# Kernel optimization log

Hardware: AMD Instinct MI355X
Metric: run time of the kernel (lower is better)

The kernel has to match this reference:

```python
import jax, jax.numpy as jnp
import numpy as np

N, IN_DIM, D, H, E, L = 50000, 16, 128, 256, 800000, 3


def setup_inputs() -> dict:
    key = jax.random.key(0)
    ks = jax.random.split(key, 32)
    s = 0.1
    inp = {
        "x": jax.random.normal(ks[0], (N, IN_DIM), dtype=jnp.float32),
        "edge_index": jax.random.randint(ks[1], (2, E), 0, N, dtype=jnp.int64),
        "enc_W": s * jax.random.normal(ks[2], (IN_DIM, D), dtype=jnp.float32),
        "enc_b": jnp.zeros((D,), jnp.float32),
        "msg_W1": s * jax.random.normal(ks[3], (L, 2 * D, H), dtype=jnp.float32),
        "msg_b1": jnp.zeros((L, H), jnp.float32),
        "msg_W2": s * jax.random.normal(ks[4], (L, H, H), dtype=jnp.float32),
        "msg_b2": jnp.zeros((L, H), jnp.float32),
        "msg_W3": s * jax.random.normal(ks[5], (L, H, D), dtype=jnp.float32),
        "msg_b3": jnp.zeros((L, D), jnp.float32),
        "gru_Wih": s * jax.random.normal(ks[6], (L, D, 3 * D), dtype=jnp.float32),
        "gru_Whh": s * jax.random.normal(ks[7], (L, D, 3 * D), dtype=jnp.float32),
        "gru_bih": jnp.zeros((L, 3 * D), jnp.float32),
        "gru_bhh": jnp.zeros((L, 3 * D), jnp.float32),
        "dec_W1": s * jax.random.normal(ks[8], (D, H), dtype=jnp.float32),
        "dec_b1": jnp.zeros((H,), jnp.float32),
        "dec_W2": s * jax.random.normal(ks[9], (H, H), dtype=jnp.float32),
        "dec_b2": jnp.zeros((H,), jnp.float32),
        "dec_W3": s * jax.random.normal(ks[10], (H, 1), dtype=jnp.float32),
        "dec_b3": jnp.zeros((1,), jnp.float32),
    }
    return inp


def reference(x, edge_index, enc_W, enc_b, msg_W1, msg_b1, msg_W2, msg_b2,
              msg_W3, msg_b3, gru_Wih, gru_Whh, gru_bih, gru_bhh,
              dec_W1, dec_b1, dec_W2, dec_b2, dec_W3, dec_b3):
    n = x.shape[0]
    d = enc_W.shape[1]
    # add self loops (PyG add_self_loops)
    loops = jnp.arange(n, dtype=edge_index.dtype)
    src = jnp.concatenate([edge_index[0], loops])  # x_j
    tgt = jnp.concatenate([edge_index[1], loops])  # x_i / aggregation bucket
    counts = jax.ops.segment_sum(jnp.ones_like(tgt, dtype=x.dtype), tgt, num_segments=n)
    # Encoder: Linear + Tanh
    h = jnp.tanh(x @ enc_W + enc_b)
    for l in range(msg_W1.shape[0]):
        # message: MLP(concat(x_i, x_j))  -> [E+N, d]
        m = jnp.concatenate([h[tgt], h[src]], axis=-1)
        m = jnp.tanh(m @ msg_W1[l] + msg_b1[l])
        m = jnp.tanh(m @ msg_W2[l] + msg_b2[l])
        m = m @ msg_W3[l] + msg_b3[l]
        # aggregate: scatter-mean into target nodes
        agg = jax.ops.segment_sum(m, tgt, num_segments=n) / counts[:, None]
        # update: GRUCell(input=agg, hidden=h)
        gi = agg @ gru_Wih[l] + gru_bih[l]
        gh = h @ gru_Whh[l] + gru_bhh[l]
        r = jax.nn.sigmoid(gi[:, :d] + gh[:, :d])
        z = jax.nn.sigmoid(gi[:, d:2 * d] + gh[:, d:2 * d])
        nn_ = jnp.tanh(gi[:, 2 * d:] + r * gh[:, 2 * d:])
        h = (1.0 - z) * nn_ + z * h
    # Decoder: Linear+Tanh, Linear+Tanh, Linear
    o = jnp.tanh(h @ dec_W1 + dec_b1)
    o = jnp.tanh(o @ dec_W2 + dec_b2)
    o = o @ dec_W3 + dec_b3  # [n, 1]
    return o[:, 0]  # x.view(-1, num_nodes).squeeze(0)
```

## Files before the change

### kernel.cpp

```cpp
#include <hip/hip_runtime.h>
#include <math.h>

#define NN 50000
#define NP 50048
#define NB 782
#define IN_DIM 16
#define DD 128
#define HH 256
#define NE 800000
#define NLAYERS 3
#define ET (NE + NN)
#define EBLK 13282

typedef unsigned short ushort_t;
typedef unsigned int uint_t;
typedef __attribute__((ext_vector_type(8))) short bf16x8;
typedef __attribute__((ext_vector_type(4))) float f32x4;

__device__ __forceinline__ float fast_tanh(float x) {
  float e = __builtin_amdgcn_exp2f(x * 2.88539008177793f);
  float r = __builtin_amdgcn_rcpf(e + 1.0f);
  return fmaf(-2.0f, r, 1.0f);
}

__device__ __forceinline__ float fast_sigmoid(float x) {
  float e = __builtin_amdgcn_exp2f(x * -1.44269504088896f);
  return __builtin_amdgcn_rcpf(e + 1.0f);
}

__device__ __forceinline__ ushort_t f2bf(float f) {
  uint_t u = __float_as_uint(f);
  u += 0x7FFFu + ((u >> 16) & 1u);
  return (ushort_t)(u >> 16);
}

__device__ __forceinline__ uint_t pack2bf(float lo, float hi) {
#if __has_builtin(__builtin_amdgcn_cvt_pk_bf16_f32)
  auto v = __builtin_amdgcn_cvt_pk_bf16_f32(lo, hi);
  uint_t r;
  __builtin_memcpy(&r, &v, 4);
  return r;
#else
  return (uint_t)f2bf(lo) | ((uint_t)f2bf(hi) << 16);
#endif
}

__device__ __forceinline__ float bflo(uint_t d) { return __uint_as_float(d << 16); }
__device__ __forceinline__ float bfhi(uint_t d) { return __uint_as_float(d & 0xFFFF0000u); }



__global__ void deg_kernel(const int* __restrict__ etgt, int* __restrict__ deg) {
  int e = blockIdx.x * blockDim.x + threadIdx.x;
  if (e >= ET) return;
  int tg = (e < NE) ? etgt[e] : (e - NE);
  atomicAdd(&deg[tg], 1);
}

__global__ __launch_bounds__(1024) void scan_kernel(const int* __restrict__ deg,
                                                    int* __restrict__ cursor,
                                                    float* __restrict__ invc) {
  __shared__ int wsum[16];
  __shared__ int carry_s;
  const int t = threadIdx.x;
  const int lane = t & 63, wid = t >> 6;
  if (t == 0) carry_s = 0;
  __syncthreads();
  for (int base = 0; base < NN; base += 1024) {
    int i = base + t;
    int d = (i < NN) ? deg[i] : 0;
    int v = d;
#pragma unroll
    for (int off = 1; off < 64; off <<= 1) {
      int u = __shfl_up(v, off);
      if (lane >= off) v += u;
    }
    if (lane == 63) wsum[wid] = v;
    __syncthreads();
    int woff = 0;
    for (int k = 0; k < wid; ++k) woff += wsum[k];
    int incl = v + woff;
    int carry = carry_s;
    __syncthreads();
    if (i < NN) {
      cursor[i] = carry + incl - d;
      invc[i] = 1.0f / (float)d;
    }
    if (t == 1023) carry_s = carry + incl;
    __syncthreads();
  }
}

__global__ void scatter_kernel(const int* __restrict__ esrc, const int* __restrict__ etgt,
                               int* __restrict__ cursor, int* __restrict__ sSrc,
                               int* __restrict__ sTgt) {
  int e = blockIdx.x * blockDim.x + threadIdx.x;
  if (e >= ET) return;
  int s, tg;
  if (e < NE) { s = esrc[e]; tg = etgt[e]; }
  else        { s = e - NE;  tg = s; }
  int pos = atomicAdd(&cursor[tg], 1);
  sSrc[pos] = s;
  sTgt[pos] = tg;
}


__global__ void encoder_kernel(const float* __restrict__ x, const float* __restrict__ W,
                               const float* __restrict__ b, float* __restrict__ h,
                               ushort_t* __restrict__ hbf) {
  int idx = blockIdx.x * blockDim.x + threadIdx.x;
  if (idx >= NN * DD) return;
  int n = idx >> 7, j = idx & (DD - 1);
  const float* xr = x + n * IN_DIM;
  float acc = b[j];
#pragma unroll
  for (int k = 0; k < IN_DIM; ++k) acc = fmaf(xr[k], W[k * DD + j], acc);
  float v = fast_tanh(acc);
  h[idx] = v;
  const int ct = (n >> 4) & 3, mr = n & 15, ks = j >> 5, q = (j >> 3) & 3, jj = j & 7;
  hbf[(size_t)(n >> 6) * 8192 + (((ct * 4 + ks) * 64) + q * 16 + mr) * 8 + jj] = f2bf(v);
}

__global__ void pack_kernel(const float* __restrict__ W, ushort_t* __restrict__ out,
                            int M, int kbsh, int ngrp, int srcStride, int outStride) {
  int tid = blockIdx.x * blockDim.x + threadIdx.x;
  if (tid >= ngrp * 64) return;
  const float* Ws = W + (size_t)blockIdx.y * srcStride;
  ushort_t* os = out + (size_t)blockIdx.y * outStride;
  int lane = tid & 63, g = tid >> 6;
  int ks = g & ((1 << kbsh) - 1);
  int rt = g >> kbsh;
  int m = rt * 16 + (lane & 15);
  int k0 = ks * 32 + ((lane >> 4) << 3);
  uint_t p[4];
#pragma unroll
  for (int d = 0; d < 4; ++d)
    p[d] = pack2bf(Ws[(size_t)(k0 + 2 * d) * M + m], Ws[(size_t)(k0 + 2 * d + 1) * M + m]);
  uint4 o;
  o.x = p[0]; o.y = p[1]; o.z = p[2]; o.w = p[3];
  *(uint4*)(os + (size_t)tid * 8) = o;
}

__global__ __launch_bounds__(256) void proj_kernel(
    const ushort_t* __restrict__ hbf, const ushort_t* __restrict__ W1p,
    const float* __restrict__ b1, ushort_t* __restrict__ Ptb, ushort_t* __restrict__ Psb) {
  const int t = threadIdx.x, blk = blockIdx.x;
  const int w = t >> 6, l = t & 63, quad = l >> 4, col = l & 15;
  const ushort_t* hb = hbf + (size_t)blk * 8192;
#pragma unroll
  for (int half = 0; half < 2; ++half) {
    f32x4 acc[4][4];
#pragma unroll
    for (int m = 0; m < 4; ++m)
#pragma unroll
      for (int ct = 0; ct < 4; ++ct) acc[m][ct] = (f32x4){0.f, 0.f, 0.f, 0.f};
#pragma unroll
    for (int ks = 0; ks < 4; ++ks) {
      bf16x8 af[4];
#pragma unroll
      for (int m = 0; m < 4; ++m)
        af[m] = *(const bf16x8*)&W1p[((size_t)((w * 4 + m) * 8 + half * 4 + ks) * 64 + l) * 8];
#pragma unroll
      for (int ct = 0; ct < 4; ++ct) {
        bf16x8 bf = *(const bf16x8*)&hb[((ct * 4 + ks) * 64 + l) * 8];
#pragma unroll
        for (int m = 0; m < 4; ++m)
          acc[m][ct] = __builtin_amdgcn_mfma_f32_16x16x32_bf16(af[m], bf, acc[m][ct], 0, 0, 0);
      }
    }
    ushort_t* out = half ? Psb : Ptb;
#pragma unroll
    for (int m = 0; m < 4; ++m) {
      const int o0 = (w * 4 + m) * 16 + quad * 4;
      f32x4 bb = (f32x4){0.f, 0.f, 0.f, 0.f};
      if (half == 0) bb = *(const f32x4*)(b1 + o0);
#pragma unroll
      for (int ct = 0; ct < 4; ++ct) {
        const size_t node = (size_t)blk * 64 + ct * 16 + col;
        uint2 d;
        d.x = pack2bf(acc[m][ct][0] + bb[0], acc[m][ct][1] + bb[1]);
        d.y = pack2bf(acc[m][ct][2] + bb[2], acc[m][ct][3] + bb[3]);
        *(uint2*)&out[node * HH + o0] = d;
      }
    }
  }
}

__global__ __launch_bounds__(256, 4) void edge_kernel(
    const int* __restrict__ sSrc, const int* __restrict__ sTgt,
    const ushort_t* __restrict__ Ptb, const ushort_t* __restrict__ Psb,
    const ushort_t* __restrict__ W2p, const float* __restrict__ b2,
    const ushort_t* __restrict__ W3p, const float* __restrict__ b3,
    const float* __restrict__ invc, float* __restrict__ agg) {
  __shared__ __align__(16) float vBf[64 * 132];
  __shared__ int sIdx[64];
  __shared__ int tIdx[64];
  ushort_t* vB = (ushort_t*)vBf;
  const int t = threadIdx.x;
  const int e0 = blockIdx.x * 64;
  if (t < 64) {
    int e = e0 + t;
    int s = 0, tg = -1;
    if (e < ET) { s = sSrc[e]; tg = sTgt[e]; }
    sIdx[t] = s;
    tIdx[t] = tg;
  }
  __syncthreads();
  {
    const int el = t & 63, c = t >> 6;
    int tg = tIdx[el]; if (tg < 0) tg = 0;
    const int s = sIdx[el];
    const uint4* pt = (const uint4*)(Ptb + (size_t)tg * HH + c * 64);
    const uint4* ps = (const uint4*)(Psb + (size_t)s * HH + c * 64);
    const int ct = el >> 4, mr = el & 15;
#pragma unroll
    for (int g = 0; g < 8; ++g) {
      uint4 av = pt[g];
      uint4 bv = ps[g];
      uint_t ad[4] = {av.x, av.y, av.z, av.w};
      uint_t bd[4] = {bv.x, bv.y, bv.z, bv.w};
      uint_t p[4];
#pragma unroll
      for (int d = 0; d < 4; ++d) {
        float flo = bflo(ad[d]) + bflo(bd[d]);
        float fhi = bfhi(ad[d]) + bfhi(bd[d]);
        p[d] = pack2bf(fast_tanh(flo), fast_tanh(fhi));
      }
      uint4 o;
      o.x = p[0]; o.y = p[1]; o.z = p[2]; o.w = p[3];
      const int ks = c * 2 + (g >> 2);
      const int quad = g & 3;
      *(uint4*)&vB[((ct * 8 + ks) * 64 + quad * 16 + mr) * 8] = o;
    }
  }
  __syncthreads();
  const int w = t >> 6, l = t & 63;
  const int quad = l >> 4, col = l & 15;
  f32x4 acc2[4][4];
#pragma unroll
  for (int rp = 0; rp < 4; ++rp)
#pragma unroll
    for (int ct = 0; ct < 4; ++ct) acc2[rp][ct] = (f32x4){0.f, 0.f, 0.f, 0.f};
#pragma unroll
  for (int ks = 0; ks < 8; ++ks) {
    bf16x8 bfrag[4];
#pragma unroll
    for (int ct = 0; ct < 4; ++ct)
      bfrag[ct] = *(const bf16x8*)&vB[((ct * 8 + ks) * 64 + l) * 8];
#pragma unroll
    for (int rp = 0; rp < 4; ++rp) {
      bf16x8 afrag = *(const bf16x8*)&W2p[((size_t)((w * 4 + rp) * 8 + ks) * 64 + l) * 8];
#pragma unroll
      for (int ct = 0; ct < 4; ++ct)
        acc2[rp][ct] = __builtin_amdgcn_mfma_f32_16x16x32_bf16(afrag, bfrag[ct], acc2[rp][ct], 0, 0, 0);
    }
  }
  __syncthreads();
#pragma unroll
  for (int rp = 0; rp < 4; ++rp) {
    f32x4 bb = *(const f32x4*)(b2 + w * 64 + rp * 16 + quad * 4);
#pragma unroll
    for (int ct = 0; ct < 4; ++ct) {
      uint2 d;
      d.x = pack2bf(fast_tanh(acc2[rp][ct][0] + bb[0]), fast_tanh(acc2[rp][ct][1] + bb[1]));
      d.y = pack2bf(fast_tanh(acc2[rp][ct][2] + bb[2]), fast_tanh(acc2[rp][ct][3] + bb[3]));
      const int gidx = (ct * 8 + w * 2 + (rp >> 1)) * 64 + ((rp & 1) * 2 + (quad >> 1)) * 16 + col;
      *(uint2*)&vB[gidx * 8 + (quad & 1) * 4] = d;
    }
  }
  __syncthreads();
  f32x4 acc3[2][4];
#pragma unroll
  for (int rp = 0; rp < 2; ++rp)
#pragma unroll
    for (int ct = 0; ct < 4; ++ct) acc3[rp][ct] = (f32x4){0.f, 0.f, 0.f, 0.f};
#pragma unroll
  for (int ks = 0; ks < 8; ++ks) {
    bf16x8 bfrag[4];
#pragma unroll
    for (int ct = 0; ct < 4; ++ct)
      bfrag[ct] = *(const bf16x8*)&vB[((ct * 8 + ks) * 64 + l) * 8];
#pragma unroll
    for (int rp = 0; rp < 2; ++rp) {
      bf16x8 afrag = *(const bf16x8*)&W3p[((size_t)((w * 2 + rp) * 8 + ks) * 64 + l) * 8];
#pragma unroll
      for (int ct = 0; ct < 4; ++ct)
        acc3[rp][ct] = __builtin_amdgcn_mfma_f32_16x16x32_bf16(afrag, bfrag[ct], acc3[rp][ct], 0, 0, 0);
    }
  }
  __syncthreads();
  {
#pragma unroll
    for (int rp = 0; rp < 2; ++rp) {
      const int m0 = w * 32 + rp * 16 + quad * 4;
      f32x4 b3v = *(const f32x4*)(b3 + m0);
#pragma unroll
      for (int ct = 0; ct < 4; ++ct) {
        float4 o4;
        o4.x = acc3[rp][ct][0] + b3v[0];
        o4.y = acc3[rp][ct][1] + b3v[1];
        o4.z = acc3[rp][ct][2] + b3v[2];
        o4.w = acc3[rp][ct][3] + b3v[3];
        *(float4*)(vBf + (ct * 16 + col) * 132 + m0) = o4;
      }
    }
  }
  __syncthreads();
  {
    const int j = t & 127;
    const int hb = t >> 7;
    const float* colp = vBf + j;
    int cur = tIdx[hb * 32];
    float a = 0.f;
    for (int e = hb * 32; e < hb * 32 + 32; ++e) {
      int tg = tIdx[e];
      if (tg != cur) {
        if (cur >= 0) atomicAdd(&agg[(size_t)cur * DD + j], a * invc[cur]);
        a = 0.f;
        cur = tg;
      }
      a += colp[e * 132];
    }
    if (cur >= 0) atomicAdd(&agg[(size_t)cur * DD + j], a * invc[cur]);
  }
}

__global__ __launch_bounds__(256, 2) void gru_kernel(
    const float* __restrict__ agg, const float* __restrict__ hg,
    const ushort_t* __restrict__ hbf_in,
    const ushort_t* __restrict__ Wihp, const ushort_t* __restrict__ Whhp,
    const float* __restrict__ bih, const float* __restrict__ bhh,
    float* __restrict__ hg_out, ushort_t* __restrict__ hbf_out,
    int doProj, const ushort_t* __restrict__ W1p, const float* __restrict__ b1,
    ushort_t* __restrict__ Ptb, ushort_t* __restrict__ Psb) {
  __shared__ __align__(16) ushort_t aggF[64 * 128];
  __shared__ __align__(16) float hT[64 * 132];
  __shared__ __align__(16) ushort_t hbfL[64 * 128];
  const int t = threadIdx.x, blk = blockIdx.x;
  const size_t nodeBase = (size_t)blk * 64;
  {
    const int row = t >> 2, c = t & 3;
    const float4* ap = (const float4*)(agg + (nodeBase + row) * DD + c * 32);
    const int ct = row >> 4, mr = row & 15;
#pragma unroll
    for (int g = 0; g < 8; ++g) {
      float4 v = ap[g];
      uint2 d;
      d.x = pack2bf(v.x, v.y);
      d.y = pack2bf(v.z, v.w);
      *(uint2*)&aggF[(((ct * 4 + c) * 64) + (g >> 1) * 16 + mr) * 8 + (g & 1) * 4] = d;
    }
    const float4* hp = (const float4*)(hg + (nodeBase + row) * DD + c * 32);
    float* hrow = hT + row * 132 + c * 32;
#pragma unroll
    for (int g = 0; g < 8; ++g) *(float4*)(hrow + g * 4) = hp[g];
  }
  __syncthreads();
  const int w = t >> 6, l = t & 63, quad = l >> 4, col = l & 15;
  const ushort_t* hbf_blk = hbf_in + nodeBase * DD;
  f32x4 bbr[2], bbz[2], bbin[2], bbhn[2];
#pragma unroll
  for (int m = 0; m < 2; ++m) {
    const int o = (w + 4 * m) * 16 + quad * 4;
    f32x4 i0 = *(const f32x4*)(bih + o),       h0 = *(const f32x4*)(bhh + o);
    f32x4 i1 = *(const f32x4*)(bih + o + 128), h1 = *(const f32x4*)(bhh + o + 128);
    bbr[m] = i0 + h0;
    bbz[m] = i1 + h1;
    bbin[m] = *(const f32x4*)(bih + o + 256);
    bbhn[m] = *(const f32x4*)(bhh + o + 256);
  }
  for (int ct = 0; ct < 4; ++ct) {
    f32x4 acc[8];
#pragma unroll
    for (int i = 0; i < 8; ++i) acc[i] = (f32x4){0.f, 0.f, 0.f, 0.f};
#pragma unroll
    for (int ks = 0; ks < 8; ++ks) {
      bf16x8 bfrag;
      if (ks < 4) bfrag = *(const bf16x8*)&aggF[((ct * 4 + ks) * 64 + l) * 8];
      else        bfrag = *(const bf16x8*)&hbf_blk[((ct * 4 + (ks - 4)) * 64 + l) * 8];
#pragma unroll
      for (int i = 0; i < 6; ++i) {
        const int rt = w + 4 * i;
        bf16x8 afrag = (ks < 4)
            ? *(const bf16x8*)&Wihp[((size_t)(rt * 4 + ks) * 64 + l) * 8]
            : *(const bf16x8*)&Whhp[((size_t)(rt * 4 + ks - 4) * 64 + l) * 8];
        const int tgt = (i < 4) ? i : ((ks < 4) ? i : i + 2);
        acc[tgt] = __builtin_amdgcn_mfma_f32_16x16x32_bf16(afrag, bfrag, acc[tgt], 0, 0, 0);
      }
    }
#pragma unroll
    for (int m = 0; m < 2; ++m) {
      const int or0 = (w + 4 * m) * 16 + quad * 4;
      float* hrow = hT + (ct * 16 + col) * 132 + or0;
      f32x4 hv = *(const f32x4*)hrow;
      f32x4 hnew;
#pragma unroll
      for (int r = 0; r < 4; ++r) {
        float rr = fast_sigmoid(acc[m][r] + bbr[m][r]);
        float zz = fast_sigmoid(acc[2 + m][r] + bbz[m][r]);
        float gin = acc[4 + m][r] + bbin[m][r];
        float ghn = acc[6 + m][r] + bbhn[m][r];
        float nn = fast_tanh(fmaf(rr, ghn, gin));
        hnew[r] = fmaf(zz, hv[r] - nn, nn);
      }
      *(f32x4*)hrow = hnew;
      uint2 d;
      d.x = pack2bf(hnew[0], hnew[1]);
      d.y = pack2bf(hnew[2], hnew[3]);
      const int ksn = 2 * m + (w >> 1);
      const int qn = 2 * (w & 1) + (quad >> 1);
      const int fidx = (((ct * 4 + ksn) * 64) + qn * 16 + col) * 8 + 4 * (quad & 1);
      *(uint2*)&hbf_out[nodeBase * DD + fidx] = d;
      *(uint2*)&hbfL[fidx] = d;
    }
  }
  __syncthreads();
  {
    const int row = t >> 2, c = t & 3;
    float* dst = hg_out + (nodeBase + row) * DD + c * 32;
    const float* src = hT + row * 132 + c * 32;
#pragma unroll
    for (int g = 0; g < 8; ++g) *(float4*)(dst + g * 4) = *(const float4*)(src + g * 4);
  }
  if (!doProj) return;
#pragma unroll
  for (int half = 0; half < 2; ++half) {
    f32x4 pacc[4][4];
#pragma unroll
    for (int m = 0; m < 4; ++m)
#pragma unroll
      for (int ct = 0; ct < 4; ++ct) pacc[m][ct] = (f32x4){0.f, 0.f, 0.f, 0.f};
#pragma unroll
    for (int ks = 0; ks < 4; ++ks) {
      bf16x8 af[4];
#pragma unroll
      for (int m = 0; m < 4; ++m)
        af[m] = *(const bf16x8*)&W1p[((size_t)((w * 4 + m) * 8 + half * 4 + ks) * 64 + l) * 8];
#pragma unroll
      for (int ct = 0; ct < 4; ++ct) {
        bf16x8 bf = *(const bf16x8*)&hbfL[((ct * 4 + ks) * 64 + l) * 8];
#pragma unroll
        for (int m = 0; m < 4; ++m)
          pacc[m][ct] = __builtin_amdgcn_mfma_f32_16x16x32_bf16(af[m], bf, pacc[m][ct], 0, 0, 0);
      }
    }
    ushort_t* outp = half ? Psb : Ptb;
#pragma unroll
    for (int m = 0; m < 4; ++m) {
      const int o0 = (w * 4 + m) * 16 + quad * 4;
      f32x4 bb = (f32x4){0.f, 0.f, 0.f, 0.f};
      if (half == 0) bb = *(const f32x4*)(b1 + o0);
#pragma unroll
      for (int ct = 0; ct < 4; ++ct) {
        const size_t node = nodeBase + ct * 16 + col;
        uint2 d;
        d.x = pack2bf(pacc[m][ct][0] + bb[0], pacc[m][ct][1] + bb[1]);
        d.y = pack2bf(pacc[m][ct][2] + bb[2], pacc[m][ct][3] + bb[3]);
        *(uint2*)&outp[node * HH + o0] = d;
      }
    }
  }
}

__global__ __launch_bounds__(256) void dec_kernel(
    const ushort_t* __restrict__ hbf, const ushort_t* __restrict__ W1p,
    const float* __restrict__ b1, const ushort_t* __restrict__ W2p,
    const float* __restrict__ b2, const float* __restrict__ w3,
    const float* __restrict__ b3, float* __restrict__ out) {
  __shared__ __align__(16) ushort_t o1F[64 * 256];
  __shared__ float red[16][64];
  const int t = threadIdx.x, blk = blockIdx.x;
  const int w = t >> 6, l = t & 63, quad = l >> 4, col = l & 15;
  const ushort_t* hb = hbf + (size_t)blk * 8192;
  {
    f32x4 a1[4][4];
#pragma unroll
    for (int m = 0; m < 4; ++m)
#pragma unroll
      for (int ct = 0; ct < 4; ++ct) a1[m][ct] = (f32x4){0.f, 0.f, 0.f, 0.f};
#pragma unroll
    for (int ks = 0; ks < 4; ++ks) {
      bf16x8 af[4];
#pragma unroll
      for (int m = 0; m < 4; ++m)
        af[m] = *(const bf16x8*)&W1p[((size_t)((w * 4 + m) * 4 + ks) * 64 + l) * 8];
#pragma unroll
      for (int ct = 0; ct < 4; ++ct) {
        bf16x8 bf = *(const bf16x8*)&hb[((ct * 4 + ks) * 64 + l) * 8];
#pragma unroll
        for (int m = 0; m < 4; ++m)
          a1[m][ct] = __builtin_amdgcn_mfma_f32_16x16x32_bf16(af[m], bf, a1[m][ct], 0, 0, 0);
      }
    }
#pragma unroll
    for (int m = 0; m < 4; ++m) {
      const int o0 = (w * 4 + m) * 16 + quad * 4;
      f32x4 bb = *(const f32x4*)(b1 + o0);
      const int ks1 = 2 * w + (m >> 1);
      const int q1 = 2 * (m & 1) + (quad >> 1);
#pragma unroll
      for (int ct = 0; ct < 4; ++ct) {
        uint2 d;
        d.x = pack2bf(fast_tanh(a1[m][ct][0] + bb[0]), fast_tanh(a1[m][ct][1] + bb[1]));
        d.y = pack2bf(fast_tanh(a1[m][ct][2] + bb[2]), fast_tanh(a1[m][ct][3] + bb[3]));
        *(uint2*)&o1F[((ct * 8 + ks1) * 64 + q1 * 16 + col) * 8 + 4 * (quad & 1)] = d;
      }
    }
  }
  __syncthreads();
  {
    f32x4 a2[4][4];
#pragma unroll
    for (int m = 0; m < 4; ++m)
#pragma unroll
      for (int ct = 0; ct < 4; ++ct) a2[m][ct] = (f32x4){0.f, 0.f, 0.f, 0.f};
#pragma unroll
    for (int ks = 0; ks < 8; ++ks) {
      bf16x8 af[4];
#pragma unroll
      for (int m = 0; m < 4; ++m)
        af[m] = *(const bf16x8*)&W2p[((size_t)((w * 4 + m) * 8 + ks) * 64 + l) * 8];
#pragma unroll
      for (int ct = 0; ct < 4; ++ct) {
        bf16x8 bf = *(const bf16x8*)&o1F[((ct * 8 + ks) * 64 + l) * 8];
#pragma unroll
        for (int m = 0; m < 4; ++m)
          a2[m][ct] = __builtin_amdgcn_mfma_f32_16x16x32_bf16(af[m], bf, a2[m][ct], 0, 0, 0);
      }
    }
    float partial[4] = {0.f, 0.f, 0.f, 0.f};
#pragma unroll
    for (int m = 0; m < 4; ++m) {
      const int o0 = (w * 4 + m) * 16 + quad * 4;
      f32x4 b2v = *(const f32x4*)(b2 + o0);
      f32x4 w3v = *(const f32x4*)(w3 + o0);
#pragma unroll
      for (int ct = 0; ct < 4; ++ct)
#pragma unroll
        for (int r = 0; r < 4; ++r)
          partial[ct] += fast_tanh(a2[m][ct][r] + b2v[r]) * w3v[r];
    }
#pragma unroll
    for (int ct = 0; ct < 4; ++ct) red[w * 4 + quad][ct * 16 + col] = partial[ct];
  }
  __syncthreads();
  if (t < 64) {
    float s = b3[0];
#pragma unroll
    for (int k = 0; k < 16; ++k) s += red[k][t];
    size_t node = (size_t)blk * 64 + t;
    if (node < NN) out[node] = s;
  }
}

extern "C" void kernel_launch(void* const* d_in, const int* in_sizes, int n_in,
                              void* d_out, int out_size, void* d_ws, size_t ws_size,
                              hipStream_t stream) {
  const float* x      = (const float*)d_in[0];
  const int*   ei     = (const int*)d_in[1];
  const float* enc_W  = (const float*)d_in[2];
  const float* enc_b  = (const float*)d_in[3];
  const float* msg_W1 = (const float*)d_in[4];
  const float* msg_b1 = (const float*)d_in[5];
  const float* msg_W2 = (const float*)d_in[6];
  const float* msg_b2 = (const float*)d_in[7];
  const float* msg_W3 = (const float*)d_in[8];
  const float* msg_b3 = (const float*)d_in[9];
  const float* gWih   = (const float*)d_in[10];
  const float* gWhh   = (const float*)d_in[11];
  const float* gbih   = (const float*)d_in[12];
  const float* gbhh   = (const float*)d_in[13];
  const float* dW1    = (const float*)d_in[14];
  const float* db1    = (const float*)d_in[15];
  const float* dW2    = (const float*)d_in[16];
  const float* db2    = (const float*)d_in[17];
  const float* dW3    = (const float*)d_in[18];
  const float* db3    = (const float*)d_in[19];
  float* out = (float*)d_out;

  float* ws = (float*)d_ws;
  float* invc = ws;
  float* h    = ws + NP;
  float* agg  = h + (size_t)NP * DD;
  ushort_t* hbfA = (ushort_t*)(agg + (size_t)NP * DD);
  ushort_t* hbfB = hbfA + (size_t)NP * DD;
  ushort_t* Ptb  = hbfB + (size_t)NP * DD;
  ushort_t* Psb  = Ptb + (size_t)NP * HH;
  ushort_t* W2pk = Psb + (size_t)NP * HH;
  ushort_t* W3pk = W2pk + 3 * 65536;
  ushort_t* W1pk = W3pk + 3 * 32768;
  ushort_t* Wihpk = W1pk + 3 * 65536;
  ushort_t* Whhpk = Wihpk + 3 * 49152;
  ushort_t* dW1pk = Whhpk + 3 * 49152;
  ushort_t* dW2pk = dW1pk + 32768;
  int* deg    = (int*)(dW2pk + 65536);
  int* cursor = deg + NP;
  int* sSrc   = cursor + NP;
  int* sTgt   = sSrc + ET;

  const int* esrc = ei;
  const int* etgt = ei + NE;

  hipMemsetAsync(deg, 0, NN * sizeof(int), stream);
  deg_kernel<<<(ET + 255) / 256, 256, 0, stream>>>(etgt, deg);
  scan_kernel<<<1, 1024, 0, stream>>>(deg, cursor, invc);
  scatter_kernel<<<(ET + 255) / 256, 256, 0, stream>>>(esrc, etgt, cursor, sSrc, sTgt);

  encoder_kernel<<<(NN * DD + 255) / 256, 256, 0, stream>>>(x, enc_W, enc_b, h, hbfA);

  pack_kernel<<<dim3(32, 3), 256, 0, stream>>>(msg_W2, W2pk, 256, 3, 128, 65536, 65536);
  pack_kernel<<<dim3(16, 3), 256, 0, stream>>>(msg_W3, W3pk, 128, 3, 64, 32768, 32768);
  pack_kernel<<<dim3(32, 3), 256, 0, stream>>>(msg_W1, W1pk, 256, 3, 128, 65536, 65536);
  pack_kernel<<<dim3(24, 3), 256, 0, stream>>>(gWih, Wihpk, 384, 2, 96, 49152, 49152);
  pack_kernel<<<dim3(24, 3), 256, 0, stream>>>(gWhh, Whhpk, 384, 2, 96, 49152, 49152);
  pack_kernel<<<dim3(16, 1), 256, 0, stream>>>(dW1, dW1pk, 256, 2, 64, 0, 0);
  pack_kernel<<<dim3(32, 1), 256, 0, stream>>>(dW2, dW2pk, 256, 3, 128, 0, 0);

  proj_kernel<<<NB, 256, 0, stream>>>(hbfA, W1pk, msg_b1, Ptb, Psb);

  for (int l = 0; l < NLAYERS; ++l) {
    const ushort_t* hin = (l & 1) ? hbfB : hbfA;
    ushort_t* hout = (l & 1) ? hbfA : hbfB;
    hipMemsetAsync(agg, 0, (size_t)NP * DD * sizeof(float), stream);
    edge_kernel<<<EBLK, 256, 0, stream>>>(
        sSrc, sTgt, Ptb, Psb, W2pk + (size_t)l * 65536, msg_b2 + (size_t)l * HH,
        W3pk + (size_t)l * 32768, msg_b3 + (size_t)l * DD, invc, agg);
    const int doProj = (l < NLAYERS - 1) ? 1 : 0;
    gru_kernel<<<NB, 256, 0, stream>>>(
        agg, h, hin, Wihpk + (size_t)l * 49152, Whhpk + (size_t)l * 49152,
        gbih + (size_t)l * 3 * DD, gbhh + (size_t)l * 3 * DD, h, hout,
        doProj, W1pk + (size_t)(l + 1) * 65536, msg_b1 + (size_t)(l + 1) * HH, Ptb, Psb);
  }
  dec_kernel<<<NB, 256, 0, stream>>>(hbfB, dW1pk, db1, dW2pk, db2, dW3, db3, out);
}
```

Measured before the change: 1.414 ms.

## Drop fp32 hidden-state copy, read GRU residual from bf16 fragments

Removes the fp32 hidden-state buffer. The encoder no longer writes it, and the GRU blend now reads the previous hidden value from the packed bf16 fragments that the MFMA step already uses. This cuts global reads and writes per layer plus a shared-memory tile, so launch bounds rise to 3 blocks per CU. The edge kernel also loads source and target indices directly per thread instead of staging them through shared memory behind a barrier. The cost is that the hidden state is carried only in bf16 across layers, which loses precision.

```diff
diff --git a/kernel.cpp b/kernel.cpp
--- a/kernel.cpp
+++ b/kernel.cpp
@@ -106,8 +106,7 @@
 
 
 __global__ void encoder_kernel(const float* __restrict__ x, const float* __restrict__ W,
-                               const float* __restrict__ b, float* __restrict__ h,
-                               ushort_t* __restrict__ hbf) {
+                               const float* __restrict__ b, ushort_t* __restrict__ hbf) {
   int idx = blockIdx.x * blockDim.x + threadIdx.x;
   if (idx >= NN * DD) return;
   int n = idx >> 7, j = idx & (DD - 1);
@@ -116,7 +115,6 @@
 #pragma unroll
   for (int k = 0; k < IN_DIM; ++k) acc = fmaf(xr[k], W[k * DD + j], acc);
   float v = fast_tanh(acc);
-  h[idx] = v;
   const int ct = (n >> 4) & 3, mr = n & 15, ks = j >> 5, q = (j >> 3) & 3, jj = j & 7;
   hbf[(size_t)(n >> 6) * 8192 + (((ct * 4 + ks) * 64) + q * 16 + mr) * 8 + jj] = f2bf(v);
 }
@@ -193,23 +191,19 @@
     const ushort_t* __restrict__ W3p, const float* __restrict__ b3,
     const float* __restrict__ invc, float* __restrict__ agg) {
   __shared__ __align__(16) float vBf[64 * 132];
-  __shared__ int sIdx[64];
   __shared__ int tIdx[64];
   ushort_t* vB = (ushort_t*)vBf;
   const int t = threadIdx.x;
   const int e0 = blockIdx.x * 64;
   if (t < 64) {
     int e = e0 + t;
-    int s = 0, tg = -1;
-    if (e < ET) { s = sSrc[e]; tg = sTgt[e]; }
-    sIdx[t] = s;
-    tIdx[t] = tg;
-  }
-  __syncthreads();
+    tIdx[t] = (e < ET) ? sTgt[e] : -1;
+  }
   {
     const int el = t & 63, c = t >> 6;
-    int tg = tIdx[el]; if (tg < 0) tg = 0;
-    const int s = sIdx[el];
+    const int eg = e0 + el;
+    int s = 0, tg = 0;
+    if (eg < ET) { s = sSrc[eg]; tg = sTgt[eg]; }
     const uint4* pt = (const uint4*)(Ptb + (size_t)tg * HH + c * 64);
     const uint4* ps = (const uint4*)(Psb + (size_t)s * HH + c * 64);
     const int ct = el >> 4, mr = el & 15;
@@ -325,16 +319,14 @@
   }
 }
 
-__global__ __launch_bounds__(256, 2) void gru_kernel(
-    const float* __restrict__ agg, const float* __restrict__ hg,
-    const ushort_t* __restrict__ hbf_in,
+__global__ __launch_bounds__(256, 3) void gru_kernel(
+    const float* __restrict__ agg, const ushort_t* __restrict__ hbf_in,
     const ushort_t* __restrict__ Wihp, const ushort_t* __restrict__ Whhp,
     const float* __restrict__ bih, const float* __restrict__ bhh,
-    float* __restrict__ hg_out, ushort_t* __restrict__ hbf_out,
+    ushort_t* __restrict__ hbf_out,
     int doProj, const ushort_t* __restrict__ W1p, const float* __restrict__ b1,
     ushort_t* __restrict__ Ptb, ushort_t* __restrict__ Psb) {
   __shared__ __align__(16) ushort_t aggF[64 * 128];
-  __shared__ __align__(16) float hT[64 * 132];
   __shared__ __align__(16) ushort_t hbfL[64 * 128];
   const int t = threadIdx.x, blk = blockIdx.x;
   const size_t nodeBase = (size_t)blk * 64;
@@ -350,10 +342,6 @@
       d.y = pack2bf(v.z, v.w);
       *(uint2*)&aggF[(((ct * 4 + c) * 64) + (g >> 1) * 16 + mr) * 8 + (g & 1) * 4] = d;
     }
-    const float4* hp = (const float4*)(hg + (nodeBase + row) * DD + c * 32);
-    float* hrow = hT + row * 132 + c * 32;
-#pragma unroll
-    for (int g = 0; g < 8; ++g) *(float4*)(hrow + g * 4) = hp[g];
   }
   __syncthreads();
   const int w = t >> 6, l = t & 63, quad = l >> 4, col = l & 15;
@@ -390,9 +378,13 @@
     }
 #pragma unroll
     for (int m = 0; m < 2; ++m) {
-      const int or0 = (w + 4 * m) * 16 + quad * 4;
-      float* hrow = hT + (ct * 16 + col) * 132 + or0;
-      f32x4 hv = *(const f32x4*)hrow;
+      const int ksn = 2 * m + (w >> 1);
+      const int qn = 2 * (w & 1) + (quad >> 1);
+      const int fidx = (((ct * 4 + ksn) * 64) + qn * 16 + col) * 8 + 4 * (quad & 1);
+      uint2 hvv = *(const uint2*)&hbf_blk[fidx];
+      f32x4 hv;
+      hv[0] = bflo(hvv.x); hv[1] = bfhi(hvv.x);
+      hv[2] = bflo(hvv.y); hv[3] = bfhi(hvv.y);
       f32x4 hnew;
 #pragma unroll
       for (int r = 0; r < 4; ++r) {
@@ -403,26 +395,15 @@
         float nn = fast_tanh(fmaf(rr, ghn, gin));
         hnew[r] = fmaf(zz, hv[r] - nn, nn);
       }
-      *(f32x4*)hrow = hnew;
       uint2 d;
       d.x = pack2bf(hnew[0], hnew[1]);
       d.y = pack2bf(hnew[2], hnew[3]);
-      const int ksn = 2 * m + (w >> 1);
-      const int qn = 2 * (w & 1) + (quad >> 1);
-      const int fidx = (((ct * 4 + ksn) * 64) + qn * 16 + col) * 8 + 4 * (quad & 1);
       *(uint2*)&hbf_out[nodeBase * DD + fidx] = d;
       *(uint2*)&hbfL[fidx] = d;
     }
   }
-  __syncthreads();
-  {
-    const int row = t >> 2, c = t & 3;
-    float* dst = hg_out + (nodeBase + row) * DD + c * 32;
-    const float* src = hT + row * 132 + c * 32;
-#pragma unroll
-    for (int g = 0; g < 8; ++g) *(float4*)(dst + g * 4) = *(const float4*)(src + g * 4);
-  }
   if (!doProj) return;
+  __syncthreads();
 #pragma unroll
   for (int half = 0; half < 2; ++half) {
     f32x4 pacc[4][4];
@@ -580,8 +561,7 @@
 
   float* ws = (float*)d_ws;
   float* invc = ws;
-  float* h    = ws + NP;
-  float* agg  = h + (size_t)NP * DD;
+  float* agg  = ws + NP;
   ushort_t* hbfA = (ushort_t*)(agg + (size_t)NP * DD);
   ushort_t* hbfB = hbfA + (size_t)NP * DD;
   ushort_t* Ptb  = hbfB + (size_t)NP * DD;
@@ -606,7 +586,7 @@
   scan_kernel<<<1, 1024, 0, stream>>>(deg, cursor, invc);
   scatter_kernel<<<(ET + 255) / 256, 256, 0, stream>>>(esrc, etgt, cursor, sSrc, sTgt);
 
-  encoder_kernel<<<(NN * DD + 255) / 256, 256, 0, stream>>>(x, enc_W, enc_b, h, hbfA);
+  encoder_kernel<<<(NN * DD + 255) / 256, 256, 0, stream>>>(x, enc_W, enc_b, hbfA);
 
   pack_kernel<<<dim3(32, 3), 256, 0, stream>>>(msg_W2, W2pk, 256, 3, 128, 65536, 65536);
   pack_kernel<<<dim3(16, 3), 256, 0, stream>>>(msg_W3, W3pk, 128, 3, 64, 32768, 32768);
@@ -627,8 +607,8 @@
         W3pk + (size_t)l * 32768, msg_b3 + (size_t)l * DD, invc, agg);
     const int doProj = (l < NLAYERS - 1) ? 1 : 0;
     gru_kernel<<<NB, 256, 0, stream>>>(
-        agg, h, hin, Wihpk + (size_t)l * 49152, Whhpk + (size_t)l * 49152,
-        gbih + (size_t)l * 3 * DD, gbhh + (size_t)l * 3 * DD, h, hout,
+        agg, hin, Wihpk + (size_t)l * 49152, Whhpk + (size_t)l * 49152,
+        gbih + (size_t)l * 3 * DD, gbhh + (size_t)l * 3 * DD, hout,
         doProj, W1pk + (size_t)(l + 1) * 65536, msg_b1 + (size_t)(l + 1) * HH, Ptb, Psb);
   }
   dec_kernel<<<NB, 256, 0, stream>>>(hbfB, dW1pk, db1, dW2pk, db2, dW3, db3, out);
```

Result: slower. 1.571 ms (+11.1%).
